# Kernel optimization log

Measured on AMD Instinct MI355X. Metric: run time of the kernel, lower is better.

The kernel has to match this reference:

```python
import jax, jax.numpy as jnp
import numpy as np

NODE_DIM = 128
DEPTH = 4
N_NODES = 10000
N_EDGES = 320000


def setup_inputs() -> dict:
    key = jax.random.key(0)
    ks = jax.random.split(key, 12)
    s = 0.05
    D = NODE_DIM
    inp = {
        'h': jax.random.normal(ks[0], (N_NODES, D), jnp.float32),
        'x': jax.random.normal(ks[1], (N_NODES, 3), jnp.float32),
        'edges': jax.random.randint(ks[2], (2, N_EDGES), 0, N_NODES, jnp.int32),
        # edge_mlp: Linear(2D+1 -> D), SiLU, Linear(D -> D), SiLU  (per layer)
        'edge_w1': jax.random.normal(ks[3], (DEPTH, 2 * D + 1, D), jnp.float32) * s,
        'edge_b1': jnp.zeros((DEPTH, D), jnp.float32),
        'edge_w2': jax.random.normal(ks[4], (DEPTH, D, D), jnp.float32) * s,
        'edge_b2': jnp.zeros((DEPTH, D), jnp.float32),
        # node_mlp: Linear(2D -> D), SiLU, Linear(D -> D)  (per layer)
        'node_w1': jax.random.normal(ks[5], (DEPTH, 2 * D, D), jnp.float32) * s,
        'node_b1': jnp.zeros((DEPTH, D), jnp.float32),
        'node_w2': jax.random.normal(ks[6], (DEPTH, D, D), jnp.float32) * s,
        'node_b2': jnp.zeros((DEPTH, D), jnp.float32),
        # coord_mlp (only used by last layer, update_coords=True):
        # Linear(D -> D), SiLU, Linear(D -> 1, bias=False)
        'coord_w1': jax.random.normal(ks[7], (D, D), jnp.float32) * s,
        'coord_b1': jnp.zeros((D,), jnp.float32),
        'coord_w2': jax.random.normal(ks[8], (D, 1), jnp.float32) * s,
    }
    return inp


def reference(h, x, edges, edge_w1, edge_b1, edge_w2, edge_b2,
              node_w1, node_b1, node_w2, node_b2,
              coord_w1, coord_b1, coord_w2):
    silu = jax.nn.silu
    row, col = edges[0], edges[1]
    n = h.shape[0]
    for i in range(DEPTH):
        # coord2radial
        coord_diff = x[row] - x[col]                       # [E, 3]
        radial = jnp.sum(coord_diff * coord_diff, axis=-1, keepdims=True)  # [E, 1]
        # edge_model: m_ij = edge_mlp([h_i, h_j, radial])
        feat = jnp.concatenate([h[row], h[col], radial], axis=-1)  # [E, 2D+1]
        m = silu(feat @ edge_w1[i] + edge_b1[i])
        m = silu(m @ edge_w2[i] + edge_b2[i])              # [E, D]
        # coord_model (only last layer, coords_agg='mean')
        if i == DEPTH - 1:
            w = silu(m @ coord_w1 + coord_b1) @ coord_w2   # [E, 1]
            trans = coord_diff * w                          # [E, 3]
            agg = jax.ops.segment_sum(trans, row, num_segments=n)
            cnt = jax.ops.segment_sum(jnp.ones((row.shape[0], 1), trans.dtype),
                                      row, num_segments=n)
            x = x + agg / jnp.maximum(cnt, 1.0)
        # node_model: h = h + node_mlp([h, sum_j m_ij])  (residual=True)
        magg = jax.ops.segment_sum(m, row, num_segments=n)  # [N, D]
        hin = jnp.concatenate([h, magg], axis=-1)           # [N, 2D]
        out = silu(hin @ node_w1[i] + node_b1[i]) @ node_w2[i] + node_b2[i]
        h = h + out
    return h, x
```

## Files before the change

kernel.cpp:

```cpp
#include <hip/hip_runtime.h>

#define NND 10000
#define NE  320000
#define DD  128
#define NDEPTH 4
#define TE  128

typedef __attribute__((ext_vector_type(8))) short s8b;
typedef __attribute__((ext_vector_type(4))) float f4;
typedef unsigned short u16;
typedef unsigned int   u32;

__device__ __forceinline__ u16 f2b(float f) {
    u32 u = __builtin_bit_cast(u32, f);
    u32 r = (u + 0x7fffu + ((u >> 16) & 1u)) >> 16;
    return (u16)r;
}

__device__ __forceinline__ float b2f(u16 b) {
    u32 u = (u32)b << 16;
    return __builtin_bit_cast(float, u);
}

__device__ __forceinline__ u32 cvt_pk(float lo, float hi) {
    u32 r;
    asm("v_cvt_pk_bf16_f32 %0, %1, %2" : "=v"(r) : "v"(lo), "v"(hi));
    return r;
}

__device__ __forceinline__ float silu_f(float v) {
    return v / (1.0f + __expf(-v));
}

__device__ __forceinline__ s8b frag_a(const u16* rowp, int g) {
    union { s8b v; uint2 u2[2]; } r;
    r.u2[0] = *(const uint2*)(rowp + 4 * g);
    r.u2[1] = *(const uint2*)(rowp + 16 + 4 * g);
    return r.v;
}

__device__ __forceinline__ f4 mfma16(s8b a, s8b b, f4 c) {
    return __builtin_amdgcn_mfma_f32_16x16x32_bf16(a, b, c, 0, 0, 0);
}

__global__ __launch_bounds__(256) void egnn_pack(
    const float* __restrict__ ew1, const float* __restrict__ ew2,
    const float* __restrict__ nw1, const float* __restrict__ nw2,
    const float* __restrict__ cw1, u16* __restrict__ pw)
{
    int t = blockIdx.x * 256 + threadIdx.x;
    if (t >= 25 * 16384) return;
    int mat = t >> 14;
    int r   = t & 16383;
    int kt  = r >> 12;
    int nt  = (r >> 9) & 7;
    int lane= (r >> 3) & 63;
    int j   = r & 7;
    int g = lane >> 4, l15 = lane & 15;
    int k = kt * 32 + ((j < 4) ? (4 * g + j) : (16 + 4 * g + (j - 4)));
    int n = nt * 16 + l15;
    float v;
    if (mat < 24) {
        int layer = mat / 6, tp = mat % 6;
        switch (tp) {
            case 0: v = ew1[((size_t)layer * 257 + k) * DD + n]; break;
            case 1: v = ew1[((size_t)layer * 257 + 128 + k) * DD + n]; break;
            case 2: v = ew2[((size_t)layer * 128 + k) * DD + n]; break;
            case 3: v = nw1[((size_t)layer * 256 + k) * DD + n]; break;
            case 4: v = nw1[((size_t)layer * 256 + 128 + k) * DD + n]; break;
            default: v = nw2[((size_t)layer * 128 + k) * DD + n]; break;
        }
    } else {
        v = cw1[(size_t)k * DD + n];
    }
    pw[t] = f2b(v);
}

__global__ __launch_bounds__(256) void egnn_init(
    const float* __restrict__ h, u16* __restrict__ hb)
{
    int i = blockIdx.x * 256 + threadIdx.x;
    size_t base = (size_t)i * 4;
    if (base >= (size_t)NND * DD) return;
    float4 v = *(const float4*)(h + base);
    union { u16 s[4]; uint2 u; } t2;
    t2.s[0] = f2b(v.x); t2.s[1] = f2b(v.y); t2.s[2] = f2b(v.z); t2.s[3] = f2b(v.w);
    *(uint2*)(hb + base) = t2.u;
}

__global__ __launch_bounds__(256) void egnn_count(
    const int* __restrict__ edges, int* __restrict__ cnts)
{
    int e = blockIdx.x * 256 + threadIdx.x;
    if (e < NE) atomicAdd(&cnts[edges[e]], 1);
}

__global__ __launch_bounds__(1024) void egnn_scan(
    const int* __restrict__ cnts, int* __restrict__ off, int* __restrict__ cursor)
{
    __shared__ int part[1024];
    const int t = threadIdx.x;
    const int base = t * 10;
    int s = 0;
    #pragma unroll
    for (int j = 0; j < 10; ++j) {
        int i = base + j;
        s += (i < NND) ? cnts[i] : 0;
    }
    part[t] = s;
    __syncthreads();
    for (int d = 1; d < 1024; d <<= 1) {
        int v = (t >= d) ? part[t - d] : 0;
        __syncthreads();
        part[t] += v;
        __syncthreads();
    }
    int run = (t == 0) ? 0 : part[t - 1];
    #pragma unroll
    for (int j = 0; j < 10; ++j) {
        int i = base + j;
        if (i <= NND) { off[i] = run; cursor[i] = run; }
        if (i < NND) run += cnts[i];
    }
}

__global__ __launch_bounds__(256) void egnn_scatter(
    const int* __restrict__ edges, int* __restrict__ cursor,
    int* __restrict__ rows, int* __restrict__ cols)
{
    int e = blockIdx.x * 256 + threadIdx.x;
    if (e >= NE) return;
    int r = edges[e];
    int p = atomicAdd(&cursor[r], 1);
    rows[p] = r;
    cols[p] = edges[NE + e];
}

__global__ __launch_bounds__(256) void egnn_pre0(
    const u16* __restrict__ hb, const u16* __restrict__ pw,
    float* __restrict__ Pb, float* __restrict__ Qb)
{
    __shared__ __attribute__((aligned(16))) u16 tH[64][136];
    const int tid = threadIdx.x;
    const int n0  = blockIdx.x * 64;

    #pragma unroll
    for (int it = 0; it < 4; ++it) {
        int idx = tid + it * 256;
        int el = idx >> 4, part = idx & 15;
        int node = n0 + el;
        if (node < NND) {
            *(uint4*)&tH[el][part * 8] = *(const uint4*)(hb + (size_t)node * DD + part * 8);
        } else {
            uint4 z = {0u, 0u, 0u, 0u};
            *(uint4*)&tH[el][part * 8] = z;
        }
    }
    __syncthreads();

    const int wv = tid >> 6, lane = tid & 63;
    const int g = lane >> 4, l15 = lane & 15;
    const int wrow = wv * 16;

    f4 accP[8], accQ[8];
    #pragma unroll
    for (int nt = 0; nt < 8; ++nt) { accP[nt] = f4{0.f,0.f,0.f,0.f}; accQ[nt] = f4{0.f,0.f,0.f,0.f}; }
    const u16* pwa = pw;
    const u16* pwb = pw + 16384;
    #pragma unroll
    for (int kt = 0; kt < 4; ++kt) {
        s8b a = frag_a(&tH[wrow + l15][kt * 32], g);
        const u16* ba = pwa + (size_t)kt * 4096 + lane * 8;
        const u16* bb = pwb + (size_t)kt * 4096 + lane * 8;
        #pragma unroll
        for (int nt = 0; nt < 8; ++nt) {
            accP[nt] = mfma16(a, *(const s8b*)(ba + nt * 512), accP[nt]);
            accQ[nt] = mfma16(a, *(const s8b*)(bb + nt * 512), accQ[nt]);
        }
    }
    #pragma unroll
    for (int nt = 0; nt < 8; ++nt) {
        int n = nt * 16 + l15;
        #pragma unroll
        for (int r = 0; r < 4; ++r) {
            int node = n0 + wrow + g * 4 + r;
            if (node < NND) {
                Pb[(size_t)node * DD + n] = accP[nt][r];
                Qb[(size_t)node * DD + n] = accQ[nt][r];
            }
        }
    }
}

__global__ __launch_bounds__(512, 4) void egnn_edge(
    const float* __restrict__ Pb, const float* __restrict__ Qb,
    const float* __restrict__ xin,
    const int* __restrict__ rows, const int* __restrict__ cols,
    const u16* __restrict__ pw,
    const float* __restrict__ ew1, const float* __restrict__ eb1,
    const float* __restrict__ eb2, const float* __restrict__ cb1,
    const float* __restrict__ cw2,
    float* __restrict__ magg, float* __restrict__ aggx,
    int layer, int last)
{
    __shared__ __attribute__((aligned(16))) u16 tA[TE][136];
    __shared__ float rad[TE];
    __shared__ float cdf[TE][3];
    __shared__ int   ridx[TE];
    __shared__ int   cidx[TE];
    __shared__ unsigned char segflag[TE + 1];

    const int tid = threadIdx.x;
    const int p0  = blockIdx.x * TE;

    if (tid < TE) {
        int p = p0 + tid;
        int r = rows[p];
        int c = cols[p];
        ridx[tid] = r; cidx[tid] = c;
        float d0 = xin[r * 3 + 0] - xin[c * 3 + 0];
        float d1 = xin[r * 3 + 1] - xin[c * 3 + 1];
        float d2 = xin[r * 3 + 2] - xin[c * 3 + 2];
        rad[tid] = d0 * d0 + d1 * d1 + d2 * d2;
        cdf[tid][0] = d0; cdf[tid][1] = d1; cdf[tid][2] = d2;
    }
    __syncthreads();

    if (tid < TE) {
        segflag[tid] = (tid == 0) || (ridx[tid] != ridx[tid - 1]);
        if (tid == 0) segflag[TE] = 1;
    }

    {
        const int cg = tid & 15;
        const int rg = tid >> 4;
        const float* b1p = eb1 + (size_t)layer * DD + cg * 8;
        const float* wrp = ew1 + ((size_t)layer * 257 + 256) * DD + cg * 8;
        float4 b0 = *(const float4*)(b1p);
        float4 b4 = *(const float4*)(b1p + 4);
        float4 w0 = *(const float4*)(wrp);
        float4 w4 = *(const float4*)(wrp + 4);
        #pragma unroll
        for (int k = 0; k < 4; ++k) {
            int row = rg + 32 * k;
            int rn = ridx[row], cn = cidx[row];
            float rd = rad[row];
            const float* pp = Pb + (size_t)rn * DD + cg * 8;
            const float* qq = Qb + (size_t)cn * DD + cg * 8;
            float4 pa = *(const float4*)(pp);
            float4 pc = *(const float4*)(pp + 4);
            float4 qa = *(const float4*)(qq);
            float4 qc = *(const float4*)(qq + 4);
            float v0 = silu_f(pa.x + qa.x + b0.x + rd * w0.x);
            float v1 = silu_f(pa.y + qa.y + b0.y + rd * w0.y);
            float v2 = silu_f(pa.z + qa.z + b0.z + rd * w0.z);
            float v3 = silu_f(pa.w + qa.w + b0.w + rd * w0.w);
            float v4 = silu_f(pc.x + qc.x + b4.x + rd * w4.x);
            float v5 = silu_f(pc.y + qc.y + b4.y + rd * w4.y);
            float v6 = silu_f(pc.z + qc.z + b4.z + rd * w4.z);
            float v7 = silu_f(pc.w + qc.w + b4.w + rd * w4.w);
            union { u32 w[4]; uint4 u; } cv;
            cv.w[0] = cvt_pk(v0, v1);
            cv.w[1] = cvt_pk(v2, v3);
            cv.w[2] = cvt_pk(v4, v5);
            cv.w[3] = cvt_pk(v6, v7);
            *(uint4*)&tA[row][cg * 8] = cv.u;
        }
    }
    __syncthreads();

    const int wv = tid >> 6, lane = tid & 63;
    const int g = lane >> 4, l15 = lane & 15;
    const int wrow = wv * 16;

    f4 acc2[8];
    #pragma unroll
    for (int nt = 0; nt < 8; ++nt) acc2[nt] = f4{0.f, 0.f, 0.f, 0.f};
    const u16* pw2 = pw + (size_t)(layer * 6 + 2) * 16384;
    #pragma unroll
    for (int kt = 0; kt < 4; ++kt) {
        s8b a = frag_a(&tA[wrow + l15][kt * 32], g);
        const u16* pb = pw2 + (size_t)kt * 4096 + lane * 8;
        #pragma unroll
        for (int nt = 0; nt < 8; ++nt) {
            s8b b = *(const s8b*)(pb + nt * 512);
            acc2[nt] = mfma16(a, b, acc2[nt]);
        }
    }
    {
        const float* b2 = eb2 + (size_t)layer * DD;
        #pragma unroll
        for (int nt = 0; nt < 8; ++nt) {
            int n = nt * 16 + l15;
            float bb = b2[n];
            #pragma unroll
            for (int r = 0; r < 4; ++r) {
                int er = wrow + g * 4 + r;
                float v = silu_f(acc2[nt][r] + bb);
                tA[er][n] = f2b(v);
            }
        }
    }
    __syncthreads();

    if (tid < 256) {
        int col  = tid & 127;
        int half = tid >> 7;
        int r0 = half * 64, r1 = r0 + 64;
        float s = 0.f;
        for (int row = r0; row < r1; ++row) {
            s += b2f(tA[row][col]);
            if (segflag[row + 1] || row == r1 - 1) {
                atomicAdd(&magg[(size_t)ridx[row] * DD + col], s);
                s = 0.f;
            }
        }
    }

    if (last) {
        f4 acc3[8];
        #pragma unroll
        for (int nt = 0; nt < 8; ++nt) acc3[nt] = f4{0.f, 0.f, 0.f, 0.f};
        const u16* pwc = pw + (size_t)24 * 16384;
        #pragma unroll
        for (int kt = 0; kt < 4; ++kt) {
            s8b a = frag_a(&tA[wrow + l15][kt * 32], g);
            const u16* pb = pwc + (size_t)kt * 4096 + lane * 8;
            #pragma unroll
            for (int nt = 0; nt < 8; ++nt) {
                s8b b = *(const s8b*)(pb + nt * 512);
                acc3[nt] = mfma16(a, b, acc3[nt]);
            }
        }
        float p[4];
        #pragma unroll
        for (int r = 0; r < 4; ++r) p[r] = 0.f;
        #pragma unroll
        for (int nt = 0; nt < 8; ++nt) {
            int n = nt * 16 + l15;
            float bb = cb1[n], w2 = cw2[n];
            #pragma unroll
            for (int r = 0; r < 4; ++r)
                p[r] += silu_f(acc3[nt][r] + bb) * w2;
        }
        #pragma unroll
        for (int off = 1; off < 16; off <<= 1) {
            #pragma unroll
            for (int r = 0; r < 4; ++r)
                p[r] += __shfl_xor(p[r], off);
        }
        if (l15 == 0) {
            #pragma unroll
            for (int r = 0; r < 4; ++r) {
                int er = wrow + 4 * g + r;
                int rn = ridx[er];
                float w = p[r];
                atomicAdd(&aggx[rn * 3 + 0], cdf[er][0] * w);
                atomicAdd(&aggx[rn * 3 + 1], cdf[er][1] * w);
                atomicAdd(&aggx[rn * 3 + 2], cdf[er][2] * w);
            }
        }
    }
}

__global__ __launch_bounds__(256) void egnn_node(
    const u16* __restrict__ hb, const float* __restrict__ resid,
    const float* __restrict__ magg, const u16* __restrict__ pw,
    const float* __restrict__ nb1, const float* __restrict__ nb2,
    float* __restrict__ out_h, u16* __restrict__ hb_out,
    float* __restrict__ Pb, float* __restrict__ Qb,
    int layer, int last)
{
    __shared__ __attribute__((aligned(16))) u16 tH[64][136];
    __shared__ __attribute__((aligned(16))) u16 tM[64][136];
    const int tid = threadIdx.x;
    const int n0  = blockIdx.x * 64;

    #pragma unroll
    for (int it = 0; it < 4; ++it) {
        int idx = tid + it * 256;
        int el = idx >> 4, part = idx & 15;
        int node = n0 + el;
        if (node < NND) {
            *(uint4*)&tH[el][part * 8] = *(const uint4*)(hb + (size_t)node * DD + part * 8);
            const float* ms = magg + (size_t)node * DD + part * 8;
            float4 m0 = *(const float4*)(ms);
            float4 m1 = *(const float4*)(ms + 4);
            union { u32 w[4]; uint4 u; } cv;
            cv.w[0] = cvt_pk(m0.x, m0.y);
            cv.w[1] = cvt_pk(m0.z, m0.w);
            cv.w[2] = cvt_pk(m1.x, m1.y);
            cv.w[3] = cvt_pk(m1.z, m1.w);
            *(uint4*)&tM[el][part * 8] = cv.u;
        } else {
            uint4 z = {0u, 0u, 0u, 0u};
            *(uint4*)&tH[el][part * 8] = z;
            *(uint4*)&tM[el][part * 8] = z;
        }
    }
    __syncthreads();

    const int wv = tid >> 6, lane = tid & 63;
    const int g = lane >> 4, l15 = lane & 15;
    const int wrow = wv * 16;

    f4 acc[8];
    #pragma unroll
    for (int nt = 0; nt < 8; ++nt) acc[nt] = f4{0.f, 0.f, 0.f, 0.f};
    const u16* pn1a = pw + (size_t)(layer * 6 + 3) * 16384;
    const u16* pn1b = pw + (size_t)(layer * 6 + 4) * 16384;
    #pragma unroll
    for (int kt = 0; kt < 8; ++kt) {
        const u16 (*tile)[136] = (kt < 4) ? tH : tM;
        const int k0 = (kt & 3) * 32;
        s8b a = frag_a(&tile[wrow + l15][k0], g);
        const u16* pb = ((kt < 4) ? pn1a : pn1b) + (size_t)(kt & 3) * 4096 + lane * 8;
        #pragma unroll
        for (int nt = 0; nt < 8; ++nt) {
            s8b b = *(const s8b*)(pb + nt * 512);
            acc[nt] = mfma16(a, b, acc[nt]);
        }
    }
    {
        const float* b1 = nb1 + (size_t)layer * DD;
        #pragma unroll
        for (int nt = 0; nt < 8; ++nt) {
            int n = nt * 16 + l15;
            float bb = b1[n];
            #pragma unroll
            for (int r = 0; r < 4; ++r) {
                int er = wrow + g * 4 + r;
                tM[er][n] = f2b(silu_f(acc[nt][r] + bb));
            }
        }
    }
    __syncthreads();

    f4 acc2[8];
    #pragma unroll
    for (int nt = 0; nt < 8; ++nt) acc2[nt] = f4{0.f, 0.f, 0.f, 0.f};
    const u16* pn2 = pw + (size_t)(layer * 6 + 5) * 16384;
    #pragma unroll
    for (int kt = 0; kt < 4; ++kt) {
        s8b a = frag_a(&tM[wrow + l15][kt * 32], g);
        const u16* pb = pn2 + (size_t)kt * 4096 + lane * 8;
        #pragma unroll
        for (int nt = 0; nt < 8; ++nt) {
            s8b b = *(const s8b*)(pb + nt * 512);
            acc2[nt] = mfma16(a, b, acc2[nt]);
        }
    }
    {
        const float* b2 = nb2 + (size_t)layer * DD;
        #pragma unroll
        for (int nt = 0; nt < 8; ++nt) {
            int n = nt * 16 + l15;
            float bb = b2[n];
            #pragma unroll
            for (int r = 0; r < 4; ++r) {
                int er = wrow + g * 4 + r;
                int node = n0 + er;
                if (node < NND) {
                    float v = acc2[nt][r] + bb + resid[(size_t)node * DD + n];
                    out_h[(size_t)node * DD + n] = v;
                    if (!last) {
                        u16 hv = f2b(v);
                        hb_out[(size_t)node * DD + n] = hv;
                        tH[er][n] = hv;
                    }
                } else if (!last) {
                    tH[er][n] = 0;
                }
            }
        }
    }

    if (!last) {
        __syncthreads();
        f4 accP[8], accQ[8];
        #pragma unroll
        for (int nt = 0; nt < 8; ++nt) { accP[nt] = f4{0.f,0.f,0.f,0.f}; accQ[nt] = f4{0.f,0.f,0.f,0.f}; }
        const u16* pwa = pw + (size_t)((layer + 1) * 6 + 0) * 16384;
        const u16* pwb = pw + (size_t)((layer + 1) * 6 + 1) * 16384;
        #pragma unroll
        for (int kt = 0; kt < 4; ++kt) {
            s8b a = frag_a(&tH[wrow + l15][kt * 32], g);
            const u16* ba = pwa + (size_t)kt * 4096 + lane * 8;
            const u16* bb = pwb + (size_t)kt * 4096 + lane * 8;
            #pragma unroll
            for (int nt = 0; nt < 8; ++nt) {
                accP[nt] = mfma16(a, *(const s8b*)(ba + nt * 512), accP[nt]);
                accQ[nt] = mfma16(a, *(const s8b*)(bb + nt * 512), accQ[nt]);
            }
        }
        #pragma unroll
        for (int nt = 0; nt < 8; ++nt) {
            int n = nt * 16 + l15;
            #pragma unroll
            for (int r = 0; r < 4; ++r) {
                int node = n0 + wrow + g * 4 + r;
                if (node < NND) {
                    Pb[(size_t)node * DD + n] = accP[nt][r];
                    Qb[(size_t)node * DD + n] = accQ[nt][r];
                }
            }
        }
    }
}

__global__ __launch_bounds__(256) void egnn_coord_out(
    const float* __restrict__ xin, const float* __restrict__ aggx,
    const int* __restrict__ off, float* __restrict__ out_x)
{
    int i = blockIdx.x * 256 + threadIdx.x;
    if (i >= NND) return;
    float c = (float)(off[i + 1] - off[i]);
    float inv = 1.0f / fmaxf(c, 1.0f);
    out_x[i * 3 + 0] = xin[i * 3 + 0] + aggx[i * 3 + 0] * inv;
    out_x[i * 3 + 1] = xin[i * 3 + 1] + aggx[i * 3 + 1] * inv;
    out_x[i * 3 + 2] = xin[i * 3 + 2] + aggx[i * 3 + 2] * inv;
}

extern "C" void kernel_launch(void* const* d_in, const int* in_sizes, int n_in,
                              void* d_out, int out_size, void* d_ws, size_t ws_size,
                              hipStream_t stream) {
    const float* h   = (const float*)d_in[0];
    const float* x   = (const float*)d_in[1];
    const int*  edges= (const int*)d_in[2];
    const float* ew1 = (const float*)d_in[3];
    const float* eb1 = (const float*)d_in[4];
    const float* ew2 = (const float*)d_in[5];
    const float* eb2 = (const float*)d_in[6];
    const float* nw1 = (const float*)d_in[7];
    const float* nb1 = (const float*)d_in[8];
    const float* nw2 = (const float*)d_in[9];
    const float* nb2 = (const float*)d_in[10];
    const float* cw1 = (const float*)d_in[11];
    const float* cb1 = (const float*)d_in[12];
    const float* cw2 = (const float*)d_in[13];

    char* ws = (char*)d_ws;
    u16*   hb   = (u16*)  (ws);
    u16*   pw   = (u16*)  (ws + 2560000);
    int*   cnts = (int*)  (ws + 3379200);
    int*   off  = (int*)  (ws + 3419216);
    int*   curs = (int*)  (ws + 3459232);
    int*   rows = (int*)  (ws + 3499248);
    int*   cols = (int*)  (ws + 4779248);
    float* aggx = (float*)(ws + 6059248);
    float* Pb   = (float*)(ws + 6179312);
    float* Qb   = (float*)(ws + 11299312);
    float* magg = (float*)(ws + 16419312);

    float* out_h = (float*)d_out;
    float* out_x = out_h + (size_t)NND * DD;

    egnn_pack<<<1600, 256, 0, stream>>>(ew1, ew2, nw1, nw2, cw1, pw);
    egnn_init<<<1250, 256, 0, stream>>>(h, hb);
    hipMemsetAsync(aggx, 0, 120064, stream);
    hipMemsetAsync(cnts, 0, 40016, stream);

    egnn_count<<<1250, 256, 0, stream>>>(edges, cnts);
    egnn_scan<<<1, 1024, 0, stream>>>(cnts, off, curs);
    egnn_scatter<<<1250, 256, 0, stream>>>(edges, curs, rows, cols);
    egnn_pre0<<<(NND + 63) / 64, 256, 0, stream>>>(hb, pw, Pb, Qb);

    for (int i = 0; i < NDEPTH; ++i) {
        int last = (i == NDEPTH - 1);
        hipMemsetAsync(magg, 0, (size_t)NND * DD * 4, stream);
        egnn_edge<<<NE / TE, 512, 0, stream>>>(Pb, Qb, x, rows, cols, pw,
                                               ew1, eb1, eb2, cb1, cw2,
                                               magg, aggx, i, last);
        const float* resid = (i == 0) ? h : (const float*)out_h;
        egnn_node<<<(NND + 63) / 64, 256, 0, stream>>>(hb, resid, magg, pw, nb1, nb2,
                                                       out_h, hb, Pb, Qb, i, last);
    }
    egnn_coord_out<<<40, 256, 0, stream>>>(x, aggx, off, out_x);
}
```

Before: 587.9 us.

## Shrink edge tile, fold bias into P, swizzle blocks, cheaper silu/bf16 convert

Halves the edge tile to 64 edges with 256-thread blocks and raises the occupancy hint. Edge blocks are remapped in an interleaved order across eight groups. The first-layer edge bias is folded into the precomputed P projection so the edge kernel no longer adds it per element. SiLU now uses a hardware reciprocal, and the software bf16 rounding is replaced by the packed convert instruction. Smaller tiles give more blocks and better latency hiding, but they also produce more segment-boundary atomics and a serial 64-row reduction per column.

New measurement: 534.6 us. 9.1% less time.

```diff
diff --git a/kernel.cpp b/kernel.cpp
--- a/kernel.cpp
+++ b/kernel.cpp
@@ -4,7 +4,7 @@
 #define NE  320000
 #define DD  128
 #define NDEPTH 4
-#define TE  128
+#define TE  64
 
 typedef __attribute__((ext_vector_type(8))) short s8b;
 typedef __attribute__((ext_vector_type(4))) float f4;
@@ -28,8 +28,12 @@
     return r;
 }
 
+__device__ __forceinline__ u16 f2b1(float v) {
+    return (u16)cvt_pk(v, v);
+}
+
 __device__ __forceinline__ float silu_f(float v) {
-    return v / (1.0f + __expf(-v));
+    return v * __builtin_amdgcn_rcpf(1.0f + __expf(-v));
 }
 
 __device__ __forceinline__ s8b frag_a(const u16* rowp, int g) {
@@ -138,6 +142,7 @@
 
 __global__ __launch_bounds__(256) void egnn_pre0(
     const u16* __restrict__ hb, const u16* __restrict__ pw,
+    const float* __restrict__ eb1,
     float* __restrict__ Pb, float* __restrict__ Qb)
 {
     __shared__ __attribute__((aligned(16))) u16 tH[64][136];
@@ -181,23 +186,24 @@
     #pragma unroll
     for (int nt = 0; nt < 8; ++nt) {
         int n = nt * 16 + l15;
+        float bb = eb1[n];
         #pragma unroll
         for (int r = 0; r < 4; ++r) {
             int node = n0 + wrow + g * 4 + r;
             if (node < NND) {
-                Pb[(size_t)node * DD + n] = accP[nt][r];
+                Pb[(size_t)node * DD + n] = accP[nt][r] + bb;
                 Qb[(size_t)node * DD + n] = accQ[nt][r];
             }
         }
     }
 }
 
-__global__ __launch_bounds__(512, 4) void egnn_edge(
+__global__ __launch_bounds__(256, 6) void egnn_edge(
     const float* __restrict__ Pb, const float* __restrict__ Qb,
     const float* __restrict__ xin,
     const int* __restrict__ rows, const int* __restrict__ cols,
     const u16* __restrict__ pw,
-    const float* __restrict__ ew1, const float* __restrict__ eb1,
+    const float* __restrict__ ew1,
     const float* __restrict__ eb2, const float* __restrict__ cb1,
     const float* __restrict__ cw2,
     float* __restrict__ magg, float* __restrict__ aggx,
@@ -211,7 +217,10 @@
     __shared__ unsigned char segflag[TE + 1];
 
     const int tid = threadIdx.x;
-    const int p0  = blockIdx.x * TE;
+    const int nblk = NE / TE;
+    const int bid  = blockIdx.x;
+    const int blk  = (bid & 7) * (nblk >> 3) + (bid >> 3);
+    const int p0   = blk * TE;
 
     if (tid < TE) {
         int p = p0 + tid;
@@ -234,15 +243,12 @@
     {
         const int cg = tid & 15;
         const int rg = tid >> 4;
-        const float* b1p = eb1 + (size_t)layer * DD + cg * 8;
         const float* wrp = ew1 + ((size_t)layer * 257 + 256) * DD + cg * 8;
-        float4 b0 = *(const float4*)(b1p);
-        float4 b4 = *(const float4*)(b1p + 4);
         float4 w0 = *(const float4*)(wrp);
         float4 w4 = *(const float4*)(wrp + 4);
         #pragma unroll
         for (int k = 0; k < 4; ++k) {
-            int row = rg + 32 * k;
+            int row = rg + 16 * k;
             int rn = ridx[row], cn = cidx[row];
             float rd = rad[row];
             const float* pp = Pb + (size_t)rn * DD + cg * 8;
@@ -251,14 +257,14 @@
             float4 pc = *(const float4*)(pp + 4);
             float4 qa = *(const float4*)(qq);
             float4 qc = *(const float4*)(qq + 4);
-            float v0 = silu_f(pa.x + qa.x + b0.x + rd * w0.x);
-            float v1 = silu_f(pa.y + qa.y + b0.y + rd * w0.y);
-            float v2 = silu_f(pa.z + qa.z + b0.z + rd * w0.z);
-            float v3 = silu_f(pa.w + qa.w + b0.w + rd * w0.w);
-            float v4 = silu_f(pc.x + qc.x + b4.x + rd * w4.x);
-            float v5 = silu_f(pc.y + qc.y + b4.y + rd * w4.y);
-            float v6 = silu_f(pc.z + qc.z + b4.z + rd * w4.z);
-            float v7 = silu_f(pc.w + qc.w + b4.w + rd * w4.w);
+            float v0 = silu_f(pa.x + qa.x + rd * w0.x);
+            float v1 = silu_f(pa.y + qa.y + rd * w0.y);
+            float v2 = silu_f(pa.z + qa.z + rd * w0.z);
+            float v3 = silu_f(pa.w + qa.w + rd * w0.w);
+            float v4 = silu_f(pc.x + qc.x + rd * w4.x);
+            float v5 = silu_f(pc.y + qc.y + rd * w4.y);
+            float v6 = silu_f(pc.z + qc.z + rd * w4.z);
+            float v7 = silu_f(pc.w + qc.w + rd * w4.w);
             union { u32 w[4]; uint4 u; } cv;
             cv.w[0] = cvt_pk(v0, v1);
             cv.w[1] = cvt_pk(v2, v3);
@@ -297,20 +303,18 @@
             for (int r = 0; r < 4; ++r) {
                 int er = wrow + g * 4 + r;
                 float v = silu_f(acc2[nt][r] + bb);
-                tA[er][n] = f2b(v);
-            }
-        }
-    }
-    __syncthreads();
-
-    if (tid < 256) {
-        int col  = tid & 127;
-        int half = tid >> 7;
-        int r0 = half * 64, r1 = r0 + 64;
+                tA[er][n] = f2b1(v);
+            }
+        }
+    }
+    __syncthreads();
+
+    if (tid < 128) {
+        int col = tid;
         float s = 0.f;
-        for (int row = r0; row < r1; ++row) {
+        for (int row = 0; row < TE; ++row) {
             s += b2f(tA[row][col]);
-            if (segflag[row + 1] || row == r1 - 1) {
+            if (segflag[row + 1] || row == TE - 1) {
                 atomicAdd(&magg[(size_t)ridx[row] * DD + col], s);
                 s = 0.f;
             }
@@ -367,6 +371,7 @@
     const u16* __restrict__ hb, const float* __restrict__ resid,
     const float* __restrict__ magg, const u16* __restrict__ pw,
     const float* __restrict__ nb1, const float* __restrict__ nb2,
+    const float* __restrict__ eb1,
     float* __restrict__ out_h, u16* __restrict__ hb_out,
     float* __restrict__ Pb, float* __restrict__ Qb,
     int layer, int last)
@@ -430,7 +435,7 @@
             #pragma unroll
             for (int r = 0; r < 4; ++r) {
                 int er = wrow + g * 4 + r;
-                tM[er][n] = f2b(silu_f(acc[nt][r] + bb));
+                tM[er][n] = f2b1(silu_f(acc[nt][r] + bb));
             }
         }
     }
@@ -464,7 +469,7 @@
                     float v = acc2[nt][r] + bb + resid[(size_t)node * DD + n];
                     out_h[(size_t)node * DD + n] = v;
                     if (!last) {
-                        u16 hv = f2b(v);
+                        u16 hv = f2b1(v);
                         hb_out[(size_t)node * DD + n] = hv;
                         tH[er][n] = hv;
                     }
@@ -496,11 +501,12 @@
         #pragma unroll
         for (int nt = 0; nt < 8; ++nt) {
             int n = nt * 16 + l15;
+            float bb = eb1[(size_t)(layer + 1) * DD + n];
             #pragma unroll
             for (int r = 0; r < 4; ++r) {
                 int node = n0 + wrow + g * 4 + r;
                 if (node < NND) {
-                    Pb[(size_t)node * DD + n] = accP[nt][r];
+                    Pb[(size_t)node * DD + n] = accP[nt][r] + bb;
                     Qb[(size_t)node * DD + n] = accQ[nt][r];
                 }
             }
@@ -563,16 +569,16 @@
     egnn_count<<<1250, 256, 0, stream>>>(edges, cnts);
     egnn_scan<<<1, 1024, 0, stream>>>(cnts, off, curs);
     egnn_scatter<<<1250, 256, 0, stream>>>(edges, curs, rows, cols);
-    egnn_pre0<<<(NND + 63) / 64, 256, 0, stream>>>(hb, pw, Pb, Qb);
+    egnn_pre0<<<(NND + 63) / 64, 256, 0, stream>>>(hb, pw, eb1, Pb, Qb);
 
     for (int i = 0; i < NDEPTH; ++i) {
         int last = (i == NDEPTH - 1);
         hipMemsetAsync(magg, 0, (size_t)NND * DD * 4, stream);
-        egnn_edge<<<NE / TE, 512, 0, stream>>>(Pb, Qb, x, rows, cols, pw,
-                                               ew1, eb1, eb2, cb1, cw2,
+        egnn_edge<<<NE / TE, 256, 0, stream>>>(Pb, Qb, x, rows, cols, pw,
+                                               ew1, eb2, cb1, cw2,
                                                magg, aggx, i, last);
         const float* resid = (i == 0) ? h : (const float*)out_h;
-        egnn_node<<<(NND + 63) / 64, 256, 0, stream>>>(hb, resid, magg, pw, nb1, nb2,
+        egnn_node<<<(NND + 63) / 64, 256, 0, stream>>>(hb, resid, magg, pw, nb1, nb2, eb1,
                                                        out_h, hb, Pb, Qb, i, last);
     }
     egnn_coord_out<<<40, 256, 0, stream>>>(x, aggx, off, out_x);
```
